# Kernel optimization log

Hardware: AMD Instinct MI355X
Metric: run time of the kernel (lower is better)

Reference implementation:

```python
import jax, jax.numpy as jnp
import numpy as np

RCUT = 6.0      # cutoff radius
AXIS = 16       # axis_neuron
NORM = 64.0     # normalizer = avg_neighbors + 1 (precomputed stat)
EPS = 1e-15
NTYPES = 2


def _embed(h, W0, b0, W1, b1, W2, b2):
    # tiny per-type-pair embedding MLP: scalar sr -> C channels
    h = jnp.tanh(h @ W0 + b0)
    h = jnp.tanh(h @ W1 + b1)
    return jnp.tanh(h @ W2 + b2)


def _forward(coord_3N, box_33, srmean, srstd, xrsrstd, Gbias, Ebias,
             emb_W0, emb_b0, emb_W1, emb_b1, emb_W2, emb_b2,
             fit_W0, fit_b0, fit_W1, fit_b1, fit_W2, fit_b2, n1):
    N = coord_3N.shape[1]
    L = jnp.diagonal(box_33)  # orthorhombic box lengths (3,)
    # relative coords with minimum-image convention: x[d,i,j] = c[d,j] - c[d,i]
    x_3NM = coord_3N[:, None, :] - coord_3N[:, :, None]
    x_3NM = x_3NM - L[:, None, None] * jnp.round(x_3NM / L[:, None, None])
    eye = jnp.eye(N, dtype=bool)
    r_NM = jnp.sqrt(jnp.where(eye, 1.0, (x_3NM ** 2).sum(0)))  # diag masked for safe grad
    # smooth switching / r  (DeepPot-SE style sr)
    u = r_NM / RCUT
    sw = jnp.where((r_NM < RCUT) & (~eye), ((-6.0 * u + 15.0) * u - 10.0) * u ** 3 + 1.0, 0.0)
    sr_NM = sw / r_NM
    rsr_NM = sr_NM / r_NM
    idx = (0, n1, N)  # contiguous type boundaries (atoms sorted by type)
    rows_sr, rows_rsr, rows_emb = [], [], []
    for i in range(NTYPES):
        sr_i = sr_NM[idx[i]:idx[i + 1]]
        rows_sr.append(sr_i / srstd[i])
        rows_rsr.append(rsr_NM[idx[i]:idx[i + 1]] / xrsrstd[i])
        srn_i = (sr_i - srmean[i]) / srstd[i]
        blocks = []
        for j in range(NTYPES):
            p = NTYPES * i + j  # type-pair index
            blocks.append(_embed(srn_i[:, idx[j]:idx[j + 1], None],
                                 emb_W0[p], emb_b0[p], emb_W1[p], emb_b1[p], emb_W2[p], emb_b2[p]))
        rows_emb.append(jnp.concatenate(blocks, axis=1))
    srbias_NM = jnp.concatenate(rows_sr, axis=0)
    R_3NM = (jnp.concatenate(rows_rsr, axis=0)[None] + EPS) * x_3NM  # e3norm = 1
    embed_NMC = jnp.concatenate(rows_emb, axis=0)
    # weighted reductions over neighbor axis M (einsum avoids the 3*N*M*C temp)
    Ginv_NC = jnp.einsum('nm,nmc->nc', srbias_NM, embed_NMC) / NORM
    Geqv_3NC = jnp.einsum('dnm,nmc->dnc', R_3NM, embed_NMC) / NORM
    G_4NC = jnp.concatenate([(Ginv_NC + Gbias)[None], Geqv_3NC], axis=0)
    # equivariant outer-product descriptor: Feat[n,a,c] = sum_k G[k,n,c]*G[k,n,a]
    Feat_NX = jnp.einsum('knc,kna->nac', G_4NC, G_4NC[:, :, :AXIS]).reshape(N, -1)
    energy = jnp.zeros((), dtype=Feat_NX.dtype)
    for i in range(NTYPES):
        h = Feat_NX[idx[i]:idx[i + 1]]
        h = jnp.tanh(h @ fit_W0[i] + fit_b0[i])
        h = jnp.tanh(h @ fit_W1[i] + fit_b1[i])
        h = h @ fit_W2[i] + fit_b2[i]
        energy = energy + (h + Ebias[i]).sum()
    return energy


def setup_inputs() -> dict:
    key = jax.random.key(0)
    ks = jax.random.split(key, 20)
    N, N1, BOXL = 1024, 512, 20.0
    W = (16, 32, 64)
    X, F = AXIS * W[-1], 128

    def wt(k, shape, fan_in):
        return jax.random.normal(k, shape, jnp.float32) / np.float32(np.sqrt(fan_in))

    return {
        'coord_3N': jax.random.uniform(ks[0], (3, N), jnp.float32) * BOXL,
        'box_33': BOXL * jnp.eye(3, dtype=jnp.float32),
        'srmean': 0.1 * jax.random.uniform(ks[1], (NTYPES,), jnp.float32),
        'srstd': 0.5 + jax.random.uniform(ks[2], (NTYPES,), jnp.float32),
        'xrsrstd': 0.5 + jax.random.uniform(ks[3], (NTYPES,), jnp.float32),
        'Gbias': 0.1 * jax.random.normal(ks[4], (W[2],), jnp.float32),
        'Ebias': jax.random.normal(ks[5], (NTYPES,), jnp.float32),
        'emb_W0': wt(ks[6], (4, 1, W[0]), 1),
        'emb_b0': 0.1 * jax.random.normal(ks[7], (4, W[0]), jnp.float32),
        'emb_W1': wt(ks[8], (4, W[0], W[1]), W[0]),
        'emb_b1': 0.1 * jax.random.normal(ks[9], (4, W[1]), jnp.float32),
        'emb_W2': wt(ks[10], (4, W[1], W[2]), W[1]),
        'emb_b2': 0.1 * jax.random.normal(ks[11], (4, W[2]), jnp.float32),
        'fit_W0': wt(ks[12], (NTYPES, X, F), X),
        'fit_b0': 0.1 * jax.random.normal(ks[13], (NTYPES, F), jnp.float32),
        'fit_W1': wt(ks[14], (NTYPES, F, F), F),
        'fit_b1': 0.1 * jax.random.normal(ks[15], (NTYPES, F), jnp.float32),
        'fit_W2': wt(ks[16], (NTYPES, F, 1), F),
        'fit_b2': 0.1 * jax.random.normal(ks[17], (NTYPES, 1), jnp.float32),
        'n1': N1,
    }


def reference(coord_3N, box_33, srmean, srstd, xrsrstd, Gbias, Ebias,
              emb_W0, emb_b0, emb_W1, emb_b1, emb_W2, emb_b2,
              fit_W0, fit_b0, fit_W1, fit_b1, fit_W2, fit_b2, n1):
    return _forward(coord_3N, box_33, srmean, srstd, xrsrstd, Gbias, Ebias,
                    emb_W0, emb_b0, emb_W1, emb_b1, emb_W2, emb_b2,
                    fit_W0, fit_b0, fit_W1, fit_b1, fit_W2, fit_b2, n1)
```

## Files before the change

### kernel.cpp

```cpp
#include <hip/hip_runtime.h>

#define RCUT 6.0f

typedef _Float16 h2 __attribute__((ext_vector_type(2)));
typedef _Float16 h8 __attribute__((ext_vector_type(8)));
typedef float    f4 __attribute__((ext_vector_type(4)));

__device__ __forceinline__ float fast_tanh(float x) {
    float e = __expf(2.0f * x);
    return 1.0f - 2.0f * __builtin_amdgcn_rcpf(e + 1.0f);
}

#if __has_builtin(__builtin_amdgcn_fdot2)
__device__ __forceinline__ float dot2(h2 a, h2 b, float c) {
    return __builtin_amdgcn_fdot2(a, b, c, false);
}
#else
__device__ __forceinline__ float dot2(h2 a, h2 b, float c) {
    return (float)a.x * (float)b.x + (float)a.y * (float)b.y + c;
}
#endif

__device__ __forceinline__ h2 pkh(float a, float b) {
#if __has_builtin(__builtin_amdgcn_cvt_pkrtz)
    union { __fp16 __attribute__((ext_vector_type(2))) r; h2 h; } u;
    u.r = __builtin_amdgcn_cvt_pkrtz(a, b);
    return u.h;
#else
    h2 r; r.x = (_Float16)a; r.y = (_Float16)b; return r;
#endif
}

__global__ __launch_bounds__(256, 4) void k_embed(
    const float* __restrict__ coord, const float* __restrict__ box,
    const float* __restrict__ srmean, const float* __restrict__ srstd,
    const float* __restrict__ xrsrstd, const float* __restrict__ Gbias,
    const float* __restrict__ eW0, const float* __restrict__ eb0,
    const float* __restrict__ eW1, const float* __restrict__ eb1,
    const float* __restrict__ eW2, const float* __restrict__ eb2,
    const int* __restrict__ n1p, h2* __restrict__ feat, int N)
{
    const int n   = blockIdx.x;
    const int tid = threadIdx.x;
    const int n1  = *n1p;
    const int ti  = (n >= n1) ? 1 : 0;

    __shared__ struct {
        float    w0[2][16], b0[2][16];
        _Float16 w1t[2][32][16];
        float    b1[2][32];
    } sw;
    __shared__ _Float16 s_h1[128][40];
    __shared__ _Float16 s_ef[4][4][64][8];
    __shared__ float s_coef[4][128];
    __shared__ unsigned short s_nbr[512];
    __shared__ float s_g4[256];
    __shared__ int   s_wcnt[4], s_wcnt0[4];

    for (int t = tid; t < 32; t += 256) { int j = t >> 4, f = t & 15;
        sw.w0[j][f] = eW0[(2 * ti + j) * 16 + f];
        sw.b0[j][f] = eb0[(2 * ti + j) * 16 + f]; }
    for (int t = tid; t < 1024; t += 256) { int j = t >> 9, r = t & 511, f = r >> 5, g = r & 31;
        sw.w1t[j][g][f] = (_Float16)eW1[(2 * ti + j) * 512 + f * 32 + g]; }
    for (int t = tid; t < 64; t += 256) { int j = t >> 5, g = t & 31;
        sw.b1[j][g] = eb1[(2 * ti + j) * 32 + g]; }

    const int wid = tid >> 6, lane = tid & 63;
    const int l15 = lane & 15, lk = lane >> 4;

    h8 bf[2][4];
    float b2r[2][4];
    #pragma unroll
    for (int j = 0; j < 2; j++) {
        const float* w2g = eW2 + (size_t)(2 * ti + j) * 2048;
        #pragma unroll
        for (int nt = 0; nt < 4; nt++) {
            h8 v;
            #pragma unroll
            for (int r = 0; r < 8; r++)
                v[r] = (_Float16)w2g[(8 * lk + r) * 64 + nt * 16 + l15];
            bf[j][nt] = v;
            b2r[j][nt] = eb2[(2 * ti + j) * 64 + nt * 16 + l15];
        }
    }

    const float Lx = box[0], Ly = box[4], Lz = box[8];
    const float iLx = 1.0f / Lx, iLy = 1.0f / Ly, iLz = 1.0f / Lz;
    const float xn = coord[n], yn = coord[N + n], zn = coord[2 * N + n];

    {
        unsigned long long bal[4];
        int wtotal = 0, wtotal0 = 0;
        const int mystart = wid * 256;
        #pragma unroll
        for (int r = 0; r < 4; r++) {
            int m = mystart + r * 64 + lane;
            float dx = coord[m] - xn;         dx -= Lx * rintf(dx * iLx);
            float dy = coord[N + m] - yn;     dy -= Ly * rintf(dy * iLy);
            float dz = coord[2 * N + m] - zn; dz -= Lz * rintf(dz * iLz);
            float r2 = dx * dx + dy * dy + dz * dz;
            bool pred = (r2 < RCUT * RCUT) && (m != n);
            bal[r] = __ballot(pred);
            unsigned long long bal0 = __ballot(pred && (m < n1));
            wtotal  += (int)__popcll(bal[r]);
            wtotal0 += (int)__popcll(bal0);
        }
        if (lane == 0) { s_wcnt[wid] = wtotal; s_wcnt0[wid] = wtotal0; }
        __syncthreads();
        int base = 0;
        for (int w = 0; w < wid; w++) base += s_wcnt[w];
        #pragma unroll
        for (int r = 0; r < 4; r++) {
            bool pred = (bal[r] >> lane) & 1ull;
            int pos = (int)__popcll(bal[r] & ((1ull << lane) - 1ull));
            if (pred && (base + pos) < 512)
                s_nbr[base + pos] = (unsigned short)(wid * 256 + r * 64 + lane);
            base += (int)__popcll(bal[r]);
        }
    }
    __syncthreads();
    int cnt  = s_wcnt[0] + s_wcnt[1] + s_wcnt[2] + s_wcnt[3];
    int cnt0 = s_wcnt0[0] + s_wcnt0[1] + s_wcnt0[2] + s_wcnt0[3];
    if (cnt > 512) cnt = 512;

    const float srm  = srmean[ti];
    const float isrs = 1.0f / srstd[ti];
    const float ixrs = 1.0f / xrsrstd[ti];

    const int p  = tid & 127;
    const int hh = tid >> 7;
    const int dummy = (n + 1 < N) ? (n + 1) : 0;

    f4 gacc = {0.0f, 0.0f, 0.0f, 0.0f};
    const f4 zf4 = {0.0f, 0.0f, 0.0f, 0.0f};

    const int ntiles = (cnt + 127) >> 7;
    for (int t = 0; t < ntiles; t++) {
        __syncthreads();
        {
            const int pi = (t << 7) + p;
            const bool valid = pi < cnt;
            int m = valid ? (int)s_nbr[pi] : dummy;
            float dx = coord[m] - xn;         dx -= Lx * rintf(dx * iLx);
            float dy = coord[N + m] - yn;     dy -= Ly * rintf(dy * iLy);
            float dz = coord[2 * N + m] - zn; dz -= Lz * rintf(dz * iLz);
            float r2 = dx * dx + dy * dy + dz * dz;
            float r  = sqrtf(r2);
            float rinv = __builtin_amdgcn_rcpf(r);
            float u  = r * (1.0f / RCUT);
            float u3 = u * u * u;
            float sw_ = ((-6.0f * u + 15.0f) * u - 10.0f) * u3 + 1.0f;
            if (!valid) sw_ = 0.0f;
            float sr  = sw_ * rinv;
            float srn = (sr - srm) * isrs;
            if (hh == 0) {
                float csr = valid ? sr * isrs : 0.0f;
                float crs = valid ? (sr * rinv * ixrs + 1e-15f) : 0.0f;
                s_coef[0][p] = csr;
                s_coef[1][p] = crs * dx;
                s_coef[2][p] = crs * dy;
                s_coef[3][p] = crs * dz;
            }

            const int j = (m >= n1) ? 1 : 0;
            float h0[16];
            #pragma unroll
            for (int f = 0; f < 16; f++)
                h0[f] = fast_tanh(fmaf(srn, sw.w0[j][f], sw.b0[j][f]));
            h2 h0p[8];
            #pragma unroll
            for (int q = 0; q < 8; q++) h0p[q] = pkh(h0[2 * q], h0[2 * q + 1]);

            #pragma unroll
            for (int q = 0; q < 8; q++) {
                float hv[2];
                #pragma unroll
                for (int u_ = 0; u_ < 2; u_++) {
                    int g = 16 * hh + 2 * q + u_;
                    union { float4 f4v; h2 h[4]; } wa, wb;
                    wa.f4v = *(const float4*)&sw.w1t[j][g][0];
                    wb.f4v = *(const float4*)&sw.w1t[j][g][8];
                    float a = sw.b1[j][g];
                    #pragma unroll
                    for (int qq = 0; qq < 4; qq++) a = dot2(h0p[qq], wa.h[qq], a);
                    #pragma unroll
                    for (int qq = 0; qq < 4; qq++) a = dot2(h0p[4 + qq], wb.h[qq], a);
                    hv[u_] = fast_tanh(a);
                }
                *(h2*)&s_h1[p][16 * hh + 2 * q] = pkh(hv[0], hv[1]);
            }
        }
        __syncthreads();

        {
            const int t128 = t << 7;
            #pragma unroll
            for (int mt2 = 0; mt2 < 2; mt2++) {
                const int mt  = 2 * wid + mt2;
                const int row = 16 * mt + l15;
                h8 a = *(const h8*)&s_h1[row][8 * lk];
                const int gpb = 16 * mt;
                const bool need0 = (t128 + gpb) < cnt0;
                const bool need1 = (t128 + gpb + 15) >= cnt0;
                #pragma unroll
                for (int nt = 0; nt < 4; nt++) {
                    f4 d0 = zf4, d1 = zf4;
                    if (need0) d0 = __builtin_amdgcn_mfma_f32_16x16x32_f16(a, bf[0][nt], zf4, 0, 0, 0);
                    if (need1) d1 = __builtin_amdgcn_mfma_f32_16x16x32_f16(a, bf[1][nt], zf4, 0, 0, 0);
                    #pragma unroll
                    for (int r = 0; r < 4; r++) {
                        int gp = gpb + 4 * lk + r;
                        bool is0 = (t128 + gp) < cnt0;
                        float dv = is0 ? d0[r] : d1[r];
                        float ev = fast_tanh(dv + (is0 ? b2r[0][nt] : b2r[1][nt]));
                        s_ef[nt][gp >> 5][l15 + 16 * ((gp & 31) >> 3)][gp & 7] = (_Float16)ev;
                    }
                }
            }
        }
        __syncthreads();

        {
            #pragma unroll
            for (int ks = 0; ks < 4; ks++) {
                h8 ac;
                #pragma unroll
                for (int r = 0; r < 8; r++) {
                    int kk = 32 * ks + 8 * lk + r;
                    float cv = (l15 < 4) ? s_coef[l15][kk] : 0.0f;
                    ac[r] = (_Float16)cv;
                }
                h8 eb = *(const h8*)&s_ef[wid][ks][lane][0];
                gacc = __builtin_amdgcn_mfma_f32_16x16x32_f16(ac, eb, gacc, 0, 0, 0);
            }
        }
    }

    if (lane < 16) {
        #pragma unroll
        for (int r = 0; r < 4; r++) {
            float gv = gacc[r] * (1.0f / 64.0f);
            if (r == 0) gv += Gbias[16 * wid + lane];
            s_g4[r * 64 + 16 * wid + lane] = gv;
        }
    }
    __syncthreads();
    {
        h2* outp = feat + (size_t)n * 512;
        #pragma unroll
        for (int q = 0; q < 2; q++) {
            int o2 = tid + 256 * q;
            int a = o2 >> 5;
            int c = (2 * o2) & 63;
            float ga0 = s_g4[a],       ga1 = s_g4[64 + a];
            float ga2 = s_g4[128 + a], ga3 = s_g4[192 + a];
            float s0 = ga0 * s_g4[c];
            s0 = fmaf(ga1, s_g4[64 + c],  s0);
            s0 = fmaf(ga2, s_g4[128 + c], s0);
            s0 = fmaf(ga3, s_g4[192 + c], s0);
            float s1 = ga0 * s_g4[c + 1];
            s1 = fmaf(ga1, s_g4[64 + c + 1],  s1);
            s1 = fmaf(ga2, s_g4[128 + c + 1], s1);
            s1 = fmaf(ga3, s_g4[192 + c + 1], s1);
            outp[o2] = pkh(s0, s1);
        }
    }
}

__global__ __launch_bounds__(256) void k_prep(
    const float* __restrict__ fW0, const float* __restrict__ fW1,
    _Float16* __restrict__ W0ht, _Float16* __restrict__ W1ht)
{
    __shared__ float s_t[32][33];
    const int b = blockIdx.x;
    const int tid = threadIdx.x;
    if (b < 256) {
        int type = b >> 7, tb = b & 127;
        int ki = tb >> 2, ci = tb & 3;
        const float* src = fW0 + (size_t)type * 131072;
        int c = tid & 31, r0 = (tid >> 5) * 4;
        #pragma unroll
        for (int q = 0; q < 4; q++)
            s_t[r0 + q][c] = src[(size_t)(ki * 32 + r0 + q) * 128 + ci * 32 + c];
        __syncthreads();
        _Float16* dst = W0ht + (size_t)type * 131072;
        int kk = tid & 31, c0 = (tid >> 5) * 4;
        #pragma unroll
        for (int q = 0; q < 4; q++)
            dst[(size_t)(ci * 32 + c0 + q) * 1024 + ki * 32 + kk] = (_Float16)s_t[kk][c0 + q];
    } else {
        int b2v = b - 256;
        int type = b2v >> 4, tb = b2v & 15;
        int ki = tb >> 2, ci = tb & 3;
        const float* src = fW1 + (size_t)type * 16384;
        int c = tid & 31, r0 = (tid >> 5) * 4;
        #pragma unroll
        for (int q = 0; q < 4; q++)
            s_t[r0 + q][c] = src[(size_t)(ki * 32 + r0 + q) * 128 + ci * 32 + c];
        __syncthreads();
        _Float16* dst = W1ht + (size_t)type * 16384;
        int kk = tid & 31, c0 = (tid >> 5) * 4;
        #pragma unroll
        for (int q = 0; q < 4; q++)
            dst[(size_t)(ci * 32 + c0 + q) * 128 + ki * 32 + kk] = (_Float16)s_t[kk][c0 + q];
    }
}

__global__ __launch_bounds__(512) void k_fit(
    const _Float16* __restrict__ featf, const _Float16* __restrict__ W0ht,
    const _Float16* __restrict__ W1ht,
    const float* __restrict__ b0, const float* __restrict__ b1,
    const float* __restrict__ W2, const float* __restrict__ b2,
    const float* __restrict__ Ebias, const int* __restrict__ n1p,
    float* __restrict__ out)
{
    __shared__ _Float16 s_A[64 * 128];
    __shared__ _Float16 s_B[128 * 128];
    __shared__ _Float16 s_h[64 * 128];
    __shared__ float s_part[8];

    const int tid  = threadIdx.x;
    const int lane = tid & 63, w = tid >> 6;
    const int mt = w >> 1, nh = w & 1;
    const int l15 = lane & 15, lk = lane >> 4;
    const int n0 = blockIdx.x * 64;
    const int n1 = *n1p;
    const int ia = (n0 >= n1) ? 1 : 0;

    const _Float16* W0t = W0ht + (size_t)ia * 131072;
    const _Float16* W1t = W1ht + (size_t)ia * 16384;

    f4 acc[4];
    #pragma unroll
    for (int nt = 0; nt < 4; nt++) acc[nt] = (f4)0.0f;

    for (int kt = 0; kt < 8; kt++) {
        __syncthreads();
        {
            int r = tid >> 3, ub = (tid & 7) * 2;
            const h8* g = (const h8*)(featf + (size_t)(n0 + r) * 1024 + kt * 128);
            #pragma unroll
            for (int q = 0; q < 2; q++) {
                int u = ub + q;
                *(h8*)&s_A[r * 128 + ((u ^ (r & 15)) << 3)] = g[u];
            }
        }
        {
            int c = tid >> 2, ub = (tid & 3) * 4;
            const h8* g = (const h8*)(W0t + (size_t)c * 1024 + kt * 128);
            #pragma unroll
            for (int q = 0; q < 4; q++) {
                int u = ub + q;
                *(h8*)&s_B[c * 128 + ((u ^ (c & 15)) << 3)] = g[u];
            }
        }
        __syncthreads();
        #pragma unroll
        for (int ks = 0; ks < 4; ks++) {
            const int row = mt * 16 + l15;
            h8 a = *(const h8*)&s_A[row * 128 + (((ks * 4 + lk) ^ (row & 15)) << 3)];
            #pragma unroll
            for (int nt = 0; nt < 4; nt++) {
                const int c = nh * 64 + nt * 16 + l15;
                h8 bfr = *(const h8*)&s_B[c * 128 + (((ks * 4 + lk) ^ (c & 15)) << 3)];
                acc[nt] = __builtin_amdgcn_mfma_f32_16x16x32_f16(a, bfr, acc[nt], 0, 0, 0);
            }
        }
    }

    #pragma unroll
    for (int nt = 0; nt < 4; nt++) {
        const int c = nh * 64 + nt * 16 + l15;
        const float bias = b0[ia * 128 + c];
        #pragma unroll
        for (int r = 0; r < 4; r++) {
            const int row = mt * 16 + lk * 4 + r;
            float v = fast_tanh(acc[nt][r] + bias);
            s_h[row * 128 + (((c >> 3) ^ (row & 15)) << 3) + (c & 7)] = (_Float16)v;
        }
    }
    __syncthreads();
    {
        int c = tid >> 2, ub = (tid & 3) * 4;
        const h8* g = (const h8*)(W1t + (size_t)c * 128);
        #pragma unroll
        for (int q = 0; q < 4; q++) {
            int u = ub + q;
            *(h8*)&s_B[c * 128 + ((u ^ (c & 15)) << 3)] = g[u];
        }
    }
    __syncthreads();

    f4 acc1[4];
    #pragma unroll
    for (int nt = 0; nt < 4; nt++) acc1[nt] = (f4)0.0f;
    #pragma unroll
    for (int ks = 0; ks < 4; ks++) {
        const int row = mt * 16 + l15;
        h8 a = *(const h8*)&s_h[row * 128 + (((ks * 4 + lk) ^ (row & 15)) << 3)];
        #pragma unroll
        for (int nt = 0; nt < 4; nt++) {
            const int c = nh * 64 + nt * 16 + l15;
            h8 bfr = *(const h8*)&s_B[c * 128 + (((ks * 4 + lk) ^ (c & 15)) << 3)];
            acc1[nt] = __builtin_amdgcn_mfma_f32_16x16x32_f16(a, bfr, acc1[nt], 0, 0, 0);
        }
    }

    float p = 0.0f;
    #pragma unroll
    for (int nt = 0; nt < 4; nt++) {
        const int c = nh * 64 + nt * 16 + l15;
        const float bias = b1[ia * 128 + c];
        const float w2v  = W2[ia * 128 + c];
        #pragma unroll
        for (int r = 0; r < 4; r++)
            p += fast_tanh(acc1[nt][r] + bias) * w2v;
    }
    #pragma unroll
    for (int m = 1; m < 64; m <<= 1) p += __shfl_xor(p, m);
    if (lane == 0) s_part[w] = p;
    __syncthreads();
    if (tid == 0) {
        float e = ((s_part[0] + s_part[1]) + (s_part[2] + s_part[3]))
                + ((s_part[4] + s_part[5]) + (s_part[6] + s_part[7]))
                + 64.0f * (b2[ia] + Ebias[ia]);
        atomicAdd(out, e);
    }
}

extern "C" void kernel_launch(void* const* d_in, const int* in_sizes, int n_in,
                              void* d_out, int out_size, void* d_ws, size_t ws_size,
                              hipStream_t stream) {
    const float* coord   = (const float*)d_in[0];
    const float* box     = (const float*)d_in[1];
    const float* srmean  = (const float*)d_in[2];
    const float* srstd   = (const float*)d_in[3];
    const float* xrsrstd = (const float*)d_in[4];
    const float* Gbias   = (const float*)d_in[5];
    const float* Ebias   = (const float*)d_in[6];
    const float* eW0     = (const float*)d_in[7];
    const float* eb0     = (const float*)d_in[8];
    const float* eW1     = (const float*)d_in[9];
    const float* eb1     = (const float*)d_in[10];
    const float* eW2     = (const float*)d_in[11];
    const float* eb2     = (const float*)d_in[12];
    const float* fW0     = (const float*)d_in[13];
    const float* fb0     = (const float*)d_in[14];
    const float* fW1     = (const float*)d_in[15];
    const float* fb1     = (const float*)d_in[16];
    const float* fW2     = (const float*)d_in[17];
    const float* fb2     = (const float*)d_in[18];
    const int*   n1p     = (const int*)d_in[19];

    const int N = in_sizes[0] / 3;
    h2* featbuf = (h2*)d_ws;
    _Float16* W0ht = (_Float16*)((char*)d_ws + (size_t)2 * 1024 * 1024);
    _Float16* W1ht = W0ht + 2 * 131072;

    (void)hipMemsetAsync(d_out, 0, sizeof(float), stream);
    k_prep<<<288, 256, 0, stream>>>(fW0, fW1, W0ht, W1ht);
    k_embed<<<N, 256, 0, stream>>>(coord, box, srmean, srstd, xrsrstd, Gbias,
                                   eW0, eb0, eW1, eb1, eW2, eb2, n1p, featbuf, N);
    k_fit<<<N / 64, 512, 0, stream>>>((const _Float16*)featbuf, W0ht, W1ht,
                                      fb0, fb1, fW2, fb2, Ebias, n1p, (float*)d_out);
}
```

Measured before the change: 47.87 us.

## Run embedding layer-1 on MFMA, fold weight prep into embed, drop memset

The second embedding layer (16->32), previously a per-thread fdot2 loop, now runs as MFMA 16x16x32 f16 tiles. The layer-0 activations are staged through a new shared buffer and type-pair selection is done by neighbor index against cnt0. The fit-weight transpose kernel is merged into k_embed as extra trailing blocks, and the output memset is replaced by a counter plus per-block slots that the last fit block sums. This removes two launches and the float atomic accumulation, at the cost of an extra barrier per tile, half-empty MFMA K lanes, and a hardcoded assumption of 16 fit blocks.

```diff
diff --git a/kernel.cpp b/kernel.cpp
--- a/kernel.cpp
+++ b/kernel.cpp
@@ -10,16 +10,6 @@
     float e = __expf(2.0f * x);
     return 1.0f - 2.0f * __builtin_amdgcn_rcpf(e + 1.0f);
 }
-
-#if __has_builtin(__builtin_amdgcn_fdot2)
-__device__ __forceinline__ float dot2(h2 a, h2 b, float c) {
-    return __builtin_amdgcn_fdot2(a, b, c, false);
-}
-#else
-__device__ __forceinline__ float dot2(h2 a, h2 b, float c) {
-    return (float)a.x * (float)b.x + (float)a.y * (float)b.y + c;
-}
-#endif
 
 __device__ __forceinline__ h2 pkh(float a, float b) {
 #if __has_builtin(__builtin_amdgcn_cvt_pkrtz)
@@ -38,32 +28,67 @@
     const float* __restrict__ eW0, const float* __restrict__ eb0,
     const float* __restrict__ eW1, const float* __restrict__ eb1,
     const float* __restrict__ eW2, const float* __restrict__ eb2,
-    const int* __restrict__ n1p, h2* __restrict__ feat, int N)
+    const int* __restrict__ n1p,
+    const float* __restrict__ fW0, const float* __restrict__ fW1,
+    h2* __restrict__ feat, _Float16* __restrict__ W0ht,
+    _Float16* __restrict__ W1ht, unsigned int* __restrict__ counter, int N)
 {
-    const int n   = blockIdx.x;
+    const int nb  = blockIdx.x;
     const int tid = threadIdx.x;
-    const int n1  = *n1p;
-    const int ti  = (n >= n1) ? 1 : 0;
-
-    __shared__ struct {
-        float    w0[2][16], b0[2][16];
-        _Float16 w1t[2][32][16];
-        float    b1[2][32];
-    } sw;
+
+    __shared__ struct { float w0[2][16], b0[2][16]; } sw;
+    __shared__ _Float16 s_h0[128][24];
     __shared__ _Float16 s_h1[128][40];
-    __shared__ _Float16 s_ef[4][4][64][8];
+    __shared__ __align__(16) _Float16 s_ef[4][4][64][8];
     __shared__ float s_coef[4][128];
     __shared__ unsigned short s_nbr[512];
     __shared__ float s_g4[256];
     __shared__ int   s_wcnt[4], s_wcnt0[4];
 
+    if (nb >= N) {
+        const int b = nb - N;
+        if (b == 0 && tid == 0) *counter = 0u;
+        float (*s_t)[33] = reinterpret_cast<float(*)[33]>(&s_ef[0][0][0][0]);
+        if (b < 256) {
+            int type = b >> 7, tb = b & 127;
+            int ki = tb >> 2, ci = tb & 3;
+            const float* src = fW0 + (size_t)type * 131072;
+            int c = tid & 31, r0 = (tid >> 5) * 4;
+            #pragma unroll
+            for (int q = 0; q < 4; q++)
+                s_t[r0 + q][c] = src[(size_t)(ki * 32 + r0 + q) * 128 + ci * 32 + c];
+            __syncthreads();
+            _Float16* dst = W0ht + (size_t)type * 131072;
+            int kk = tid & 31, c0 = (tid >> 5) * 4;
+            #pragma unroll
+            for (int q = 0; q < 4; q++)
+                dst[(size_t)(ci * 32 + c0 + q) * 1024 + ki * 32 + kk] = (_Float16)s_t[kk][c0 + q];
+        } else {
+            int b2v = b - 256;
+            int type = b2v >> 4, tb = b2v & 15;
+            int ki = tb >> 2, ci = tb & 3;
+            const float* src = fW1 + (size_t)type * 16384;
+            int c = tid & 31, r0 = (tid >> 5) * 4;
+            #pragma unroll
+            for (int q = 0; q < 4; q++)
+                s_t[r0 + q][c] = src[(size_t)(ki * 32 + r0 + q) * 128 + ci * 32 + c];
+            __syncthreads();
+            _Float16* dst = W1ht + (size_t)type * 16384;
+            int kk = tid & 31, c0 = (tid >> 5) * 4;
+            #pragma unroll
+            for (int q = 0; q < 4; q++)
+                dst[(size_t)(ci * 32 + c0 + q) * 128 + ki * 32 + kk] = (_Float16)s_t[kk][c0 + q];
+        }
+        return;
+    }
+
+    const int n  = nb;
+    const int n1 = *n1p;
+    const int ti = (n >= n1) ? 1 : 0;
+
     for (int t = tid; t < 32; t += 256) { int j = t >> 4, f = t & 15;
         sw.w0[j][f] = eW0[(2 * ti + j) * 16 + f];
         sw.b0[j][f] = eb0[(2 * ti + j) * 16 + f]; }
-    for (int t = tid; t < 1024; t += 256) { int j = t >> 9, r = t & 511, f = r >> 5, g = r & 31;
-        sw.w1t[j][g][f] = (_Float16)eW1[(2 * ti + j) * 512 + f * 32 + g]; }
-    for (int t = tid; t < 64; t += 256) { int j = t >> 5, g = t & 31;
-        sw.b1[j][g] = eb1[(2 * ti + j) * 32 + g]; }
 
     const int wid = tid >> 6, lane = tid & 63;
     const int l15 = lane & 15, lk = lane >> 4;
@@ -81,6 +106,23 @@
                 v[r] = (_Float16)w2g[(8 * lk + r) * 64 + nt * 16 + l15];
             bf[j][nt] = v;
             b2r[j][nt] = eb2[(2 * ti + j) * 64 + nt * 16 + l15];
+        }
+    }
+    h8 w1f[2][2];
+    float b1r[2][2];
+    #pragma unroll
+    for (int j = 0; j < 2; j++) {
+        const float* w1g = eW1 + (size_t)(2 * ti + j) * 512;
+        #pragma unroll
+        for (int nt1 = 0; nt1 < 2; nt1++) {
+            h8 v = {};
+            if (lk < 2) {
+                #pragma unroll
+                for (int r = 0; r < 8; r++)
+                    v[r] = (_Float16)w1g[(8 * lk + r) * 32 + 16 * nt1 + l15];
+            }
+            w1f[j][nt1] = v;
+            b1r[j][nt1] = eb1[(2 * ti + j) * 32 + 16 * nt1 + l15];
         }
     }
 
@@ -136,9 +178,10 @@
 
     const int ntiles = (cnt + 127) >> 7;
     for (int t = 0; t < ntiles; t++) {
-        __syncthreads();
-        {
-            const int pi = (t << 7) + p;
+        const int t128 = t << 7;
+        __syncthreads();
+        {
+            const int pi = t128 + p;
             const bool valid = pi < cnt;
             int m = valid ? (int)s_nbr[pi] : dummy;
             float dx = coord[m] - xn;         dx -= Lx * rintf(dx * iLx);
@@ -161,39 +204,46 @@
                 s_coef[2][p] = crs * dy;
                 s_coef[3][p] = crs * dz;
             }
-
             const int j = (m >= n1) ? 1 : 0;
-            float h0[16];
-            #pragma unroll
-            for (int f = 0; f < 16; f++)
-                h0[f] = fast_tanh(fmaf(srn, sw.w0[j][f], sw.b0[j][f]));
-            h2 h0p[8];
-            #pragma unroll
-            for (int q = 0; q < 8; q++) h0p[q] = pkh(h0[2 * q], h0[2 * q + 1]);
-
+            h8 v;
             #pragma unroll
             for (int q = 0; q < 8; q++) {
-                float hv[2];
+                int f = 8 * hh + q;
+                v[q] = (_Float16)fast_tanh(fmaf(srn, sw.w0[j][f], sw.b0[j][f]));
+            }
+            *(h8*)&s_h0[p][8 * hh] = v;
+        }
+        __syncthreads();
+
+        {
+            #pragma unroll
+            for (int mt2 = 0; mt2 < 2; mt2++) {
+                const int mt  = 2 * wid + mt2;
+                const int row = 16 * mt + l15;
+                h8 a = {};
+                if (lk < 2) a = *(const h8*)&s_h0[row][8 * lk];
+                const int gpb = 16 * mt;
+                const bool need0 = (t128 + gpb) < cnt0;
+                const bool need1 = (t128 + gpb + 15) >= cnt0;
                 #pragma unroll
-                for (int u_ = 0; u_ < 2; u_++) {
-                    int g = 16 * hh + 2 * q + u_;
-                    union { float4 f4v; h2 h[4]; } wa, wb;
-                    wa.f4v = *(const float4*)&sw.w1t[j][g][0];
-                    wb.f4v = *(const float4*)&sw.w1t[j][g][8];
-                    float a = sw.b1[j][g];
+                for (int nt1 = 0; nt1 < 2; nt1++) {
+                    f4 d0 = zf4, d1 = zf4;
+                    if (need0) d0 = __builtin_amdgcn_mfma_f32_16x16x32_f16(a, w1f[0][nt1], zf4, 0, 0, 0);
+                    if (need1) d1 = __builtin_amdgcn_mfma_f32_16x16x32_f16(a, w1f[1][nt1], zf4, 0, 0, 0);
                     #pragma unroll
-                    for (int qq = 0; qq < 4; qq++) a = dot2(h0p[qq], wa.h[qq], a);
-                    #pragma unroll
-                    for (int qq = 0; qq < 4; qq++) a = dot2(h0p[4 + qq], wb.h[qq], a);
-                    hv[u_] = fast_tanh(a);
+                    for (int r = 0; r < 4; r++) {
+                        int gp = gpb + 4 * lk + r;
+                        bool is0 = (t128 + gp) < cnt0;
+                        float dv = is0 ? d0[r] : d1[r];
+                        float hv = fast_tanh(dv + (is0 ? b1r[0][nt1] : b1r[1][nt1]));
+                        s_h1[gp][16 * nt1 + l15] = (_Float16)hv;
+                    }
                 }
-                *(h2*)&s_h1[p][16 * hh + 2 * q] = pkh(hv[0], hv[1]);
-            }
-        }
-        __syncthreads();
-
-        {
-            const int t128 = t << 7;
+            }
+        }
+        __syncthreads();
+
+        {
             #pragma unroll
             for (int mt2 = 0; mt2 < 2; mt2++) {
                 const int mt  = 2 * wid + mt2;
@@ -267,51 +317,13 @@
     }
 }
 
-__global__ __launch_bounds__(256) void k_prep(
-    const float* __restrict__ fW0, const float* __restrict__ fW1,
-    _Float16* __restrict__ W0ht, _Float16* __restrict__ W1ht)
-{
-    __shared__ float s_t[32][33];
-    const int b = blockIdx.x;
-    const int tid = threadIdx.x;
-    if (b < 256) {
-        int type = b >> 7, tb = b & 127;
-        int ki = tb >> 2, ci = tb & 3;
-        const float* src = fW0 + (size_t)type * 131072;
-        int c = tid & 31, r0 = (tid >> 5) * 4;
-        #pragma unroll
-        for (int q = 0; q < 4; q++)
-            s_t[r0 + q][c] = src[(size_t)(ki * 32 + r0 + q) * 128 + ci * 32 + c];
-        __syncthreads();
-        _Float16* dst = W0ht + (size_t)type * 131072;
-        int kk = tid & 31, c0 = (tid >> 5) * 4;
-        #pragma unroll
-        for (int q = 0; q < 4; q++)
-            dst[(size_t)(ci * 32 + c0 + q) * 1024 + ki * 32 + kk] = (_Float16)s_t[kk][c0 + q];
-    } else {
-        int b2v = b - 256;
-        int type = b2v >> 4, tb = b2v & 15;
-        int ki = tb >> 2, ci = tb & 3;
-        const float* src = fW1 + (size_t)type * 16384;
-        int c = tid & 31, r0 = (tid >> 5) * 4;
-        #pragma unroll
-        for (int q = 0; q < 4; q++)
-            s_t[r0 + q][c] = src[(size_t)(ki * 32 + r0 + q) * 128 + ci * 32 + c];
-        __syncthreads();
-        _Float16* dst = W1ht + (size_t)type * 16384;
-        int kk = tid & 31, c0 = (tid >> 5) * 4;
-        #pragma unroll
-        for (int q = 0; q < 4; q++)
-            dst[(size_t)(ci * 32 + c0 + q) * 128 + ki * 32 + kk] = (_Float16)s_t[kk][c0 + q];
-    }
-}
-
 __global__ __launch_bounds__(512) void k_fit(
     const _Float16* __restrict__ featf, const _Float16* __restrict__ W0ht,
     const _Float16* __restrict__ W1ht,
     const float* __restrict__ b0, const float* __restrict__ b1,
     const float* __restrict__ W2, const float* __restrict__ b2,
     const float* __restrict__ Ebias, const int* __restrict__ n1p,
+    unsigned int* __restrict__ counter, float* __restrict__ slots,
     float* __restrict__ out)
 {
     __shared__ _Float16 s_A[64 * 128];
@@ -424,7 +436,17 @@
         float e = ((s_part[0] + s_part[1]) + (s_part[2] + s_part[3]))
                 + ((s_part[4] + s_part[5]) + (s_part[6] + s_part[7]))
                 + 64.0f * (b2[ia] + Ebias[ia]);
-        atomicAdd(out, e);
+        slots[blockIdx.x] = e;
+        __threadfence();
+        unsigned int old = atomicAdd(counter, 1u);
+        if (old == 15u) {
+            __threadfence();
+            float tot = 0.0f;
+            #pragma unroll
+            for (int i = 0; i < 16; i++)
+                tot += __hip_atomic_load(&slots[i], __ATOMIC_RELAXED, __HIP_MEMORY_SCOPE_AGENT);
+            out[0] = tot;
+        }
     }
 }
 
@@ -453,14 +475,17 @@
     const int*   n1p     = (const int*)d_in[19];
 
     const int N = in_sizes[0] / 3;
-    h2* featbuf = (h2*)d_ws;
+    h2*       featbuf = (h2*)d_ws;
     _Float16* W0ht = (_Float16*)((char*)d_ws + (size_t)2 * 1024 * 1024);
     _Float16* W1ht = W0ht + 2 * 131072;
-
-    (void)hipMemsetAsync(d_out, 0, sizeof(float), stream);
-    k_prep<<<288, 256, 0, stream>>>(fW0, fW1, W0ht, W1ht);
-    k_embed<<<N, 256, 0, stream>>>(coord, box, srmean, srstd, xrsrstd, Gbias,
-                                   eW0, eb0, eW1, eb1, eW2, eb2, n1p, featbuf, N);
+    char* tail = (char*)d_ws + (size_t)(2 * 1024 + 512 + 64) * 1024;
+    unsigned int* counter = (unsigned int*)tail;
+    float*        slots   = (float*)(tail + 64);
+
+    k_embed<<<N + 288, 256, 0, stream>>>(coord, box, srmean, srstd, xrsrstd, Gbias,
+                                         eW0, eb0, eW1, eb1, eW2, eb2, n1p,
+                                         fW0, fW1, featbuf, W0ht, W1ht, counter, N);
     k_fit<<<N / 64, 512, 0, stream>>>((const _Float16*)featbuf, W0ht, W1ht,
-                                      fb0, fb1, fW2, fb2, Ebias, n1p, (float*)d_out);
+                                      fb0, fb1, fW2, fb2, Ebias, n1p,
+                                      counter, slots, (float*)d_out);
 }
```

After: 41.04 us. -14.3%, faster.
